# Kernel tuning notes

Measured on AMD Instinct MI355X. Metric: run time of the kernel, lower is better.

## Reference

```python
import jax, jax.numpy as jnp
import numpy as np

DIN = 512      # input feature dim (din)
HEADS = 8
DHEAD = 64
DIM = HEADS * DHEAD  # 512
NTOT = 12288   # total nodes across all graphs
NBATCH = 32    # number of graphs
NMAX = 512     # padded max nodes per graph (<= pf_threshold ~562 -> softmax branch)
EPS = 1e-5


def setup_inputs() -> dict:
    key = jax.random.key(0)
    ks = jax.random.split(key, 7)
    z = jax.random.normal(ks[0], (NTOT, DIN), jnp.float32)
    src = jnp.sort(jax.random.randint(ks[1], (NTOT,), 0, NBATCH)).astype(jnp.int32)
    w_scale = 1.0 / np.sqrt(DIN)
    Wq = jax.random.normal(ks[2], (DIN, DIM), jnp.float32) * w_scale
    Wk = jax.random.normal(ks[3], (DIN, DIM), jnp.float32) * w_scale
    Wv = jax.random.normal(ks[4], (DIN, DIM), jnp.float32) * w_scale
    Wo = jax.random.normal(ks[5], (DIM, DIM), jnp.float32) * w_scale
    bo = jnp.zeros((DIM,), jnp.float32)
    ln_gamma = jnp.ones((DIN,), jnp.float32)
    ln_beta = jnp.zeros((DIN,), jnp.float32)
    return {"z": z, "src": src, "ln_gamma": ln_gamma, "ln_beta": ln_beta,
            "Wq": Wq, "Wk": Wk, "Wv": Wv, "Wo": Wo, "bo": bo,
            "n_max": NMAX, "n_batch": NBATCH}


def reference(z, src, ln_gamma, ln_beta, Wq, Wk, Wv, Wo, bo, n_max, n_batch):
    # --- LayerNorm(din) ---
    mu = jnp.mean(z, axis=-1, keepdims=True)
    var = jnp.mean(jnp.square(z - mu), axis=-1, keepdims=True)
    zn = (z - mu) * jax.lax.rsqrt(var + EPS) * ln_gamma + ln_beta

    # --- to_dense_batch(zn, src): src is sorted graph-id per node ---
    ntot = z.shape[0]
    counts = jnp.bincount(src, length=n_batch)                    # [B]
    starts = jnp.concatenate([jnp.zeros((1,), counts.dtype), jnp.cumsum(counts)[:-1]])
    pos = jnp.arange(ntot) - starts[src]                          # position within graph
    x = jnp.zeros((n_batch, n_max, DIN), zn.dtype).at[src, pos].set(zn)   # [B,N,din]
    mask = jnp.zeros((n_batch, n_max), bool).at[src, pos].set(True)       # [B,N]

    # --- q/k/v projections, split heads: b n (h d) -> b h n d ---
    def heads(t):
        return t.reshape(n_batch, n_max, HEADS, DHEAD).transpose(0, 2, 1, 3)
    q = heads(x @ Wq)
    k = heads(x @ Wk)
    v = heads(x @ Wv)

    # --- manual masked softmax attention (N <= pf_threshold branch) ---
    s = jnp.einsum('bhmd,bhnd->bhmn', q, k)
    s = jnp.where(mask[:, None, None, :], s, -jnp.inf)
    a = jax.nn.softmax(s * (DHEAD ** -0.5), axis=-1)
    o = jnp.einsum('bhmn,bhnd->bhmd', a, v)

    # --- merge heads, gather valid rows (out[mask]), output projection ---
    o = o.transpose(0, 2, 1, 3).reshape(n_batch, n_max, DIM)
    h = o[src, pos] @ Wo + bo                                     # [Ntot, DIM]
    return h
```

## Files before the change

### kernel.cpp

```cpp
#include <hip/hip_runtime.h>
#include <hip/hip_bf16.h>
#include <math.h>

#define DIN 512
#define DIM 512
#define NHEADS 8
#define DHEAD 64
#define NB 32
#define NPAD 512
#define NPTOT (NB * NPAD)

typedef __attribute__((ext_vector_type(8))) short bf16x8;
typedef __attribute__((ext_vector_type(8))) unsigned short u16x8;
typedef __attribute__((ext_vector_type(4))) float f32x4;

typedef __attribute__((address_space(3))) unsigned int lds_u32;
typedef __attribute__((address_space(1))) const unsigned int g_u32;

__device__ __forceinline__ void gll16(const unsigned short* g, unsigned short* l) {
  __builtin_amdgcn_global_load_lds((g_u32*)g, (lds_u32*)l, 16, 0, 0);
}

__device__ inline unsigned short f2bf(float x) {
  unsigned int u = __float_as_uint(x);
  unsigned int r = (u + 0x7FFFu + ((u >> 16) & 1u)) >> 16;
  return (unsigned short)r;
}

__global__ __launch_bounds__(256) void prep_kernel(const float* __restrict__ z,
                                                   const float* __restrict__ gamma,
                                                   const float* __restrict__ beta,
                                                   const int* __restrict__ src,
                                                   const float* __restrict__ Wq,
                                                   const float* __restrict__ Wk,
                                                   const float* __restrict__ Wv,
                                                   const float* __restrict__ Wo,
                                                   unsigned short* __restrict__ zn,
                                                   int* __restrict__ starts,
                                                   int* __restrict__ dstrow,
                                                   unsigned short* __restrict__ WtQKV,
                                                   unsigned short* __restrict__ WtO,
                                                   int ntot) {
  __shared__ float tile[32][33];
  int b = blockIdx.x;
  int nln = ntot >> 2;
  int nmap = (ntot + 255) >> 8;
  if (b < nln) {
    int wave = b * 4 + (threadIdx.x >> 6);
    int lane = threadIdx.x & 63;
    const float* row = z + (size_t)wave * DIN;
    float4 a = ((const float4*)row)[lane];
    float4 bb = ((const float4*)row)[64 + lane];
    float s  = a.x + a.y + a.z + a.w + bb.x + bb.y + bb.z + bb.w;
    float sq = a.x*a.x + a.y*a.y + a.z*a.z + a.w*a.w
             + bb.x*bb.x + bb.y*bb.y + bb.z*bb.z + bb.w*bb.w;
#pragma unroll
    for (int off = 32; off; off >>= 1) {
      s  += __shfl_xor(s, off);
      sq += __shfl_xor(sq, off);
    }
    float mu  = s * (1.0f / DIN);
    float var = sq * (1.0f / DIN) - mu * mu;
    float r   = rsqrtf(var + 1e-5f);
    float4 g0 = ((const float4*)gamma)[lane];
    float4 g1 = ((const float4*)gamma)[64 + lane];
    float4 b0 = ((const float4*)beta)[lane];
    float4 b1 = ((const float4*)beta)[64 + lane];
    ushort4 o0, o1;
    o0.x = f2bf((a.x - mu) * r * g0.x + b0.x);
    o0.y = f2bf((a.y - mu) * r * g0.y + b0.y);
    o0.z = f2bf((a.z - mu) * r * g0.z + b0.z);
    o0.w = f2bf((a.w - mu) * r * g0.w + b0.w);
    o1.x = f2bf((bb.x - mu) * r * g1.x + b1.x);
    o1.y = f2bf((bb.y - mu) * r * g1.y + b1.y);
    o1.z = f2bf((bb.z - mu) * r * g1.z + b1.z);
    o1.w = f2bf((bb.w - mu) * r * g1.w + b1.w);
    ((ushort4*)(zn + (size_t)wave * DIN))[lane] = o0;
    ((ushort4*)(zn + (size_t)wave * DIN))[64 + lane] = o1;
  } else if (b < nln + nmap) {
    int bid = b - nln;
    if (bid == 0 && threadIdx.x <= NB) {
      int gg = threadIdx.x;
      int lo = 0, hi = ntot;
      while (lo < hi) { int mid = (lo + hi) >> 1; if (src[mid] < gg) lo = mid + 1; else hi = mid; }
      starts[gg] = lo;
    }
    int i = bid * 256 + threadIdx.x;
    if (i < ntot) {
      int gg = src[i];
      int lo = 0, hi = ntot;
      while (lo < hi) { int mid = (lo + hi) >> 1; if (src[mid] < gg) lo = mid + 1; else hi = mid; }
      dstrow[i] = gg * NPAD + (i - lo);
    }
  } else {
    int idx = b - nln - nmap;
    int zz = idx >> 8;
    int rem = idx & 255;
    const float* W; unsigned short* Wt;
    if (zz == 0)      { W = Wq; Wt = WtQKV; }
    else if (zz == 1) { W = Wk; Wt = WtQKV + (size_t)512 * DIN; }
    else if (zz == 2) { W = Wv; Wt = WtQKV + (size_t)1024 * DIN; }
    else              { W = Wo; Wt = WtO; }
    int k0 = (rem & 15) * 32;
    int n0 = (rem >> 4) * 32;
    int tx = threadIdx.x & 31;
    int ty = threadIdx.x >> 5;
#pragma unroll
    for (int i = 0; i < 4; i++)
      tile[ty + i * 8][tx] = W[(size_t)(k0 + ty + i * 8) * DIM + n0 + tx];
    __syncthreads();
#pragma unroll
    for (int i = 0; i < 4; i++)
      Wt[(size_t)(n0 + ty + i * 8) * DIN + k0 + tx] = f2bf(tile[tx][ty + i * 8]);
  }
}

template <int NCOLS, bool BIAS, bool OUT_F32, bool REMAP>
__global__ __launch_bounds__(256) void gemm_staged(const unsigned short* __restrict__ A,
                                                   const unsigned short* __restrict__ Bt,
                                                   const float* __restrict__ bias,
                                                   const int* __restrict__ remap,
                                                   unsigned short* __restrict__ Cbf,
                                                   float* __restrict__ Cf) {
  __shared__ unsigned short smem[16384];
  int tid = threadIdx.x, lane = tid & 63, wv = tid >> 6;
  int col = lane & 15, quad = lane >> 4;
  int m0 = blockIdx.x * 128, n0 = blockIdx.y * 128;
  int msub = (wv & 1) * 64, nsub = (wv >> 1) * 64;

  int srow = lane >> 2;
  int cswz = (((lane & 3) ^ ((lane >> 3) & 3))) * 8;

  f32x4 acc[4][4];
#pragma unroll
  for (int i = 0; i < 4; i++)
#pragma unroll
    for (int j = 0; j < 4; j++) acc[i][j] = (f32x4){0.f, 0.f, 0.f, 0.f};

  auto stage = [&](int ks, int nb) {
    const unsigned short* Ab = A  + (size_t)m0 * DIN + ks * 32;
    const unsigned short* Bb = Bt + (size_t)n0 * DIN + ks * 32;
#pragma unroll
    for (int i = 0; i < 2; i++) {
      int t = wv * 2 + i;
      gll16(Ab + (size_t)(t * 16 + srow) * DIN + cswz, smem + nb * 4096 + t * 512);
      gll16(Bb + (size_t)(t * 16 + srow) * DIN + cswz, smem + 8192 + nb * 4096 + t * 512);
    }
  };

  stage(0, 0);
#pragma unroll 2
  for (int ks = 0; ks < 16; ks++) {
    int cur = ks & 1;
    __syncthreads();
    if (ks + 1 < 16) stage(ks + 1, 1 - cur);
    bf16x8 af[4], bfr[4];
#pragma unroll
    for (int mt = 0; mt < 4; mt++) {
      int row = msub + mt * 16 + col;
      af[mt] = *(const bf16x8*)&smem[cur * 4096 + row * 32 + ((quad ^ ((row >> 1) & 3)) * 8)];
    }
#pragma unroll
    for (int nt = 0; nt < 4; nt++) {
      int row = nsub + nt * 16 + col;
      bfr[nt] = *(const bf16x8*)&smem[8192 + cur * 4096 + row * 32 + ((quad ^ ((row >> 1) & 3)) * 8)];
    }
#pragma unroll
    for (int mt = 0; mt < 4; mt++)
#pragma unroll
      for (int nt = 0; nt < 4; nt++)
        acc[mt][nt] = __builtin_amdgcn_mfma_f32_16x16x32_bf16(af[mt], bfr[nt], acc[mt][nt], 0, 0, 0);
  }

  if (!OUT_F32) {
    __syncthreads();
#pragma unroll
    for (int mt = 0; mt < 4; mt++)
#pragma unroll
      for (int r = 0; r < 4; r++) {
        int row = msub + mt * 16 + quad * 4 + r;
#pragma unroll
        for (int nt = 0; nt < 4; nt++) {
          int c = nsub + nt * 16 + col;
          float v = acc[mt][nt][r] + (BIAS ? bias[n0 + c] : 0.f);
          smem[row * 128 + (((c >> 3) ^ (quad << 1)) * 8) + (c & 7)] = f2bf(v);
        }
      }
    __syncthreads();
#pragma unroll
    for (int pass = 0; pass < 8; pass++) {
      int row = pass * 16 + (tid >> 4);
      int sw  = ((row >> 2) & 3) << 1;
      int ch  = tid & 15;
      u16x8 vv = *(const u16x8*)&smem[row * 128 + ((ch ^ sw) * 8)];
      int drow = REMAP ? remap[m0 + row] : (m0 + row);
      *(u16x8*)(Cbf + (size_t)drow * NCOLS + n0 + ch * 8) = vv;
    }
  } else {
    float* smemf = (float*)smem;
    float bv[4];
#pragma unroll
    for (int nt = 0; nt < 4; nt++) bv[nt] = BIAS ? bias[n0 + nsub + nt * 16 + col] : 0.f;
#pragma unroll
    for (int hh = 0; hh < 2; hh++) {
      __syncthreads();
      if ((wv & 1) == hh) {
#pragma unroll
        for (int mt = 0; mt < 4; mt++)
#pragma unroll
          for (int r = 0; r < 4; r++) {
            int row64 = mt * 16 + quad * 4 + r;
#pragma unroll
            for (int nt = 0; nt < 4; nt++) {
              int c = nsub + nt * 16 + col;
              smemf[row64 * 128 + (c ^ (quad * 16))] = acc[mt][nt][r] + bv[nt];
            }
          }
      }
      __syncthreads();
#pragma unroll
      for (int p = 0; p < 2; p++) {
        int row64 = p * 32 + (tid >> 3);
        int sub = tid & 7;
        int sw = ((row64 >> 2) & 3) * 16;
#pragma unroll
        for (int i = 0; i < 4; i++) {
          int c = sub * 4 + i * 32;
          f32x4 v4 = *(const f32x4*)&smemf[row64 * 128 + (c ^ sw)];
          *(f32x4*)&Cf[(size_t)(m0 + hh * 64 + row64) * NCOLS + n0 + c] = v4;
        }
      }
    }
  }
}

__global__ __launch_bounds__(256, 3) void fattn_kernel(const unsigned short* __restrict__ qkvp,
                                                       const int* __restrict__ starts,
                                                       unsigned short* __restrict__ obuf) {
  __shared__ unsigned short Kbuf[2][64 * 64];
  __shared__ unsigned short Vbuf[2][64 * 64];
  __shared__ unsigned short Plds[4][32 * 64];
  int g = blockIdx.x, h = blockIdx.y, qt = blockIdx.z;
  int st = starts[g];
  int n  = starts[g + 1] - st;
  int q0b = qt * 128;
  if (q0b >= n) return;
  int tid = threadIdx.x, lane = tid & 63, wv = tid >> 6;
  int col = lane & 15, quad = lane >> 4;
  int q0 = q0b + wv * 32;
  bool active = q0 < n;
  int ntiles = (n + 63) >> 6;

  bf16x8 qf[2][2];
  if (active) {
#pragma unroll
    for (int a = 0; a < 2; a++) {
      const unsigned short* qp = qkvp + (size_t)(g * NPAD + q0 + a * 16 + col) * 1536 + h * 64 + quad * 8;
      qf[a][0] = *(const bf16x8*)(qp);
      qf[a][1] = *(const bf16x8*)(qp + 32);
    }
  }

  int srow = tid >> 2;
  int sc   = (tid & 3) * 2;
  int kwoff0 = srow * 64 + ((sc ^ (srow & 7)) * 8);
  int kwoff1 = srow * 64 + (((sc + 1) ^ (srow & 7)) * 8);
  int vkp = tid >> 3;
  int vdc = tid & 7;
  int vkc   = vkp >> 2;
  int vkoff = (vkp & 3) * 2;
  u16x8 kreg0, kreg1, vreg0, vreg1;
  auto loadregs = [&](int kt) {
    const unsigned short* kp = qkvp + (size_t)(g * NPAD + kt + srow) * 1536 + 512 + h * 64 + sc * 8;
    kreg0 = *(const u16x8*)(kp);
    kreg1 = *(const u16x8*)(kp + 8);
    const unsigned short* vp = qkvp + (size_t)(g * NPAD + kt + 2 * vkp) * 1536 + 1024 + h * 64 + vdc * 8;
    vreg0 = *(const u16x8*)(vp);
    vreg1 = *(const u16x8*)(vp + 1536);
  };
  auto writelds = [&](int bsel) {
    *(u16x8*)&Kbuf[bsel][kwoff0] = kreg0;
    *(u16x8*)&Kbuf[bsel][kwoff1] = kreg1;
#pragma unroll
    for (int i = 0; i < 8; i++) {
      int d = vdc * 8 + i;
      unsigned int pv = (unsigned int)(unsigned short)vreg0[i]
                      | ((unsigned int)(unsigned short)vreg1[i] << 16);
      *(unsigned int*)&Vbuf[bsel][d * 64 + ((vkc ^ (d & 7) ^ (d >> 3)) * 8) + vkoff] = pv;
    }
  };

  bf16x8 onesv;
#pragma unroll
  for (int i = 0; i < 8; i++) onesv[i] = (short)0x3F80;

  f32x4 oa[2][4];
  f32x4 lacc[2];
#pragma unroll
  for (int a = 0; a < 2; a++) {
    lacc[a] = (f32x4){0.f, 0.f, 0.f, 0.f};
#pragma unroll
    for (int i = 0; i < 4; i++) oa[a][i] = (f32x4){0.f, 0.f, 0.f, 0.f};
  }

  loadregs(0);
  writelds(0);
  __syncthreads();

  for (int t = 0; t < ntiles; t++) {
    int cur = t & 1;
    if (t + 1 < ntiles) loadregs((t + 1) * 64);
    if (active) {
      f32x4 s[2][4];
#pragma unroll
      for (int a = 0; a < 2; a++)
#pragma unroll
        for (int j = 0; j < 4; j++) s[a][j] = (f32x4){0.f, 0.f, 0.f, 0.f};
#pragma unroll
      for (int j = 0; j < 4; j++) {
        int R = j * 16 + col;
        bf16x8 kf0 = *(const bf16x8*)&Kbuf[cur][R * 64 + ((quad ^ (R & 7)) * 8)];
        bf16x8 kf1 = *(const bf16x8*)&Kbuf[cur][R * 64 + (((4 + quad) ^ (R & 7)) * 8)];
        s[0][j] = __builtin_amdgcn_mfma_f32_16x16x32_bf16(qf[0][0], kf0, s[0][j], 0, 0, 0);
        s[0][j] = __builtin_amdgcn_mfma_f32_16x16x32_bf16(qf[0][1], kf1, s[0][j], 0, 0, 0);
        s[1][j] = __builtin_amdgcn_mfma_f32_16x16x32_bf16(qf[1][0], kf0, s[1][j], 0, 0, 0);
        s[1][j] = __builtin_amdgcn_mfma_f32_16x16x32_bf16(qf[1][1], kf1, s[1][j], 0, 0, 0);
      }
      int kt = t * 64;
#pragma unroll
      for (int j = 0; j < 4; j++) {
        bool valid = (kt + j * 16 + col) < n;
#pragma unroll
        for (int a = 0; a < 2; a++)
#pragma unroll
          for (int r = 0; r < 4; r++)
            s[a][j][r] = valid ? __expf(s[a][j][r] * 0.125f) : 0.f;
      }
#pragma unroll
      for (int a = 0; a < 2; a++)
#pragma unroll
        for (int r = 0; r < 4; r++) {
          int R = a * 16 + quad * 4 + r;
#pragma unroll
          for (int j = 0; j < 4; j++) {
            int chunk = j * 2 + (col >> 3);
            Plds[wv][R * 64 + ((chunk ^ (R & 7)) * 8) + (col & 7)] = f2bf(s[a][j][r]);
          }
        }
      __builtin_amdgcn_fence(__ATOMIC_ACQ_REL, "workgroup");
      bf16x8 pf[2][2];
#pragma unroll
      for (int a = 0; a < 2; a++) {
        int R = a * 16 + col;
        pf[a][0] = *(const bf16x8*)&Plds[wv][R * 64 + ((quad ^ (col & 7)) * 8)];
        pf[a][1] = *(const bf16x8*)&Plds[wv][R * 64 + (((4 + quad) ^ (col & 7)) * 8)];
      }
#pragma unroll
      for (int dt = 0; dt < 4; dt++) {
        int R = dt * 16 + col;
        int swz = (R & 7) ^ (R >> 3);
        bf16x8 vf0 = *(const bf16x8*)&Vbuf[cur][R * 64 + ((quad ^ swz) * 8)];
        bf16x8 vf1 = *(const bf16x8*)&Vbuf[cur][R * 64 + (((quad + 4) ^ swz) * 8)];
        oa[0][dt] = __builtin_amdgcn_mfma_f32_16x16x32_bf16(pf[0][0], vf0, oa[0][dt], 0, 0, 0);
        oa[0][dt] = __builtin_amdgcn_mfma_f32_16x16x32_bf16(pf[0][1], vf1, oa[0][dt], 0, 0, 0);
        oa[1][dt] = __builtin_amdgcn_mfma_f32_16x16x32_bf16(pf[1][0], vf0, oa[1][dt], 0, 0, 0);
        oa[1][dt] = __builtin_amdgcn_mfma_f32_16x16x32_bf16(pf[1][1], vf1, oa[1][dt], 0, 0, 0);
      }
      lacc[0] = __builtin_amdgcn_mfma_f32_16x16x32_bf16(pf[0][0], onesv, lacc[0], 0, 0, 0);
      lacc[0] = __builtin_amdgcn_mfma_f32_16x16x32_bf16(pf[0][1], onesv, lacc[0], 0, 0, 0);
      lacc[1] = __builtin_amdgcn_mfma_f32_16x16x32_bf16(pf[1][0], onesv, lacc[1], 0, 0, 0);
      lacc[1] = __builtin_amdgcn_mfma_f32_16x16x32_bf16(pf[1][1], onesv, lacc[1], 0, 0, 0);
    }
    if (t + 1 < ntiles) writelds(1 - cur);
    __syncthreads();
  }

  if (active) {
#pragma unroll
    for (int a = 0; a < 2; a++)
#pragma unroll
      for (int r = 0; r < 4; r++) {
        int q = q0 + a * 16 + quad * 4 + r;
        if (q < n) {
          float inv = 1.0f / lacc[a][r];
          unsigned short* op = obuf + (size_t)(st + q) * DIM + h * 64 + col;
          op[0]  = f2bf(oa[a][0][r] * inv);
          op[16] = f2bf(oa[a][1][r] * inv);
          op[32] = f2bf(oa[a][2][r] * inv);
          op[48] = f2bf(oa[a][3][r] * inv);
        }
      }
  }
}

extern "C" void kernel_launch(void* const* d_in, const int* in_sizes, int n_in,
                              void* d_out, int out_size, void* d_ws, size_t ws_size,
                              hipStream_t stream) {
  const float* z     = (const float*)d_in[0];
  const int*   src   = (const int*)d_in[1];
  const float* gamma = (const float*)d_in[2];
  const float* beta  = (const float*)d_in[3];
  const float* Wq    = (const float*)d_in[4];
  const float* Wk    = (const float*)d_in[5];
  const float* Wv    = (const float*)d_in[6];
  const float* Wo    = (const float*)d_in[7];
  const float* bo    = (const float*)d_in[8];
  int ntot = in_sizes[0] / DIN;
  float* out = (float*)d_out;

  char* ws = (char*)d_ws;
  size_t off = 0;
  unsigned short* zn    = (unsigned short*)(ws + off); off += (size_t)ntot * DIN * 2;
  unsigned short* qkvp  = (unsigned short*)(ws + off); off += (size_t)NPTOT * 1536 * 2;
  unsigned short* obuf  = (unsigned short*)(ws + off); off += (size_t)ntot * DIM * 2;
  unsigned short* WtQKV = (unsigned short*)(ws + off); off += (size_t)1536 * DIN * 2;
  unsigned short* WtO   = (unsigned short*)(ws + off); off += (size_t)DIM * DIN * 2;
  int* starts           = (int*)(ws + off);            off += 64 * 4;
  int* dstrow           = (int*)(ws + off);

  int nln = ntot >> 2;
  int nmap = (ntot + 255) >> 8;
  prep_kernel<<<nln + nmap + 1024, 256, 0, stream>>>(z, gamma, beta, src, Wq, Wk, Wv, Wo,
                                                     zn, starts, dstrow, WtQKV, WtO, ntot);

  gemm_staged<1536, false, false, true>
      <<<dim3(ntot / 128, 12), 256, 0, stream>>>(zn, WtQKV, nullptr, dstrow, qkvp, nullptr);

  fattn_kernel<<<dim3(NB, NHEADS, 4), 256, 0, stream>>>(qkvp, starts, obuf);

  gemm_staged<512, true, true, false>
      <<<dim3(ntot / 128, 4), 256, 0, stream>>>(obuf, WtO, bo, nullptr, nullptr, out);
}
```

Before: 173.0 us.

## Retile QKV GEMM to 128x192 tiles and split out-proj GEMM into 128x64 tiles

The templated GEMM is split into two specialized kernels. The QKV projection now uses 128x192 tiles, giving 768 blocks instead of 1152 and more B reuse per A load, with the epilogue writing bf16 output in three 64-column passes through LDS. The output projection uses narrower 128x64 tiles, doubling its grid to 768 blocks for better CU occupancy, and writes fp32 results straight from registers instead of staging them in LDS. The trade-offs are higher register pressure in the QKV kernel and less coalesced direct stores in the output kernel.

Result: slower. 185.8 us (+7.4%).

```diff
diff --git a/kernel.cpp b/kernel.cpp
--- a/kernel.cpp
+++ b/kernel.cpp
@@ -115,36 +115,37 @@
   }
 }
 
-template <int NCOLS, bool BIAS, bool OUT_F32, bool REMAP>
-__global__ __launch_bounds__(256) void gemm_staged(const unsigned short* __restrict__ A,
+__global__ __launch_bounds__(256, 3) void gemm_qkv(const unsigned short* __restrict__ A,
                                                    const unsigned short* __restrict__ Bt,
-                                                   const float* __restrict__ bias,
                                                    const int* __restrict__ remap,
-                                                   unsigned short* __restrict__ Cbf,
-                                                   float* __restrict__ Cf) {
-  __shared__ unsigned short smem[16384];
+                                                   unsigned short* __restrict__ Cbf) {
+  __shared__ unsigned short smem[20480];
   int tid = threadIdx.x, lane = tid & 63, wv = tid >> 6;
   int col = lane & 15, quad = lane >> 4;
-  int m0 = blockIdx.x * 128, n0 = blockIdx.y * 128;
-  int msub = (wv & 1) * 64, nsub = (wv >> 1) * 64;
+  int m0 = blockIdx.x * 128, n0 = blockIdx.y * 192;
+  int msub = (wv & 1) * 64, nsub = (wv >> 1) * 96;
 
   int srow = lane >> 2;
   int cswz = (((lane & 3) ^ ((lane >> 3) & 3))) * 8;
 
-  f32x4 acc[4][4];
+  f32x4 acc[4][6];
 #pragma unroll
   for (int i = 0; i < 4; i++)
 #pragma unroll
-    for (int j = 0; j < 4; j++) acc[i][j] = (f32x4){0.f, 0.f, 0.f, 0.f};
+    for (int j = 0; j < 6; j++) acc[i][j] = (f32x4){0.f, 0.f, 0.f, 0.f};
 
   auto stage = [&](int ks, int nb) {
     const unsigned short* Ab = A  + (size_t)m0 * DIN + ks * 32;
     const unsigned short* Bb = Bt + (size_t)n0 * DIN + ks * 32;
 #pragma unroll
-    for (int i = 0; i < 2; i++) {
-      int t = wv * 2 + i;
-      gll16(Ab + (size_t)(t * 16 + srow) * DIN + cswz, smem + nb * 4096 + t * 512);
-      gll16(Bb + (size_t)(t * 16 + srow) * DIN + cswz, smem + 8192 + nb * 4096 + t * 512);
+    for (int i = 0; i < 5; i++) {
+      int t = i * 4 + wv;
+      if (t < 8)
+        gll16(Ab + (size_t)(t * 16 + srow) * DIN + cswz, smem + nb * 4096 + t * 512);
+      else {
+        int tb = t - 8;
+        gll16(Bb + (size_t)(tb * 16 + srow) * DIN + cswz, smem + 8192 + nb * 6144 + tb * 512);
+      }
     }
   };
 
@@ -154,84 +155,123 @@
     int cur = ks & 1;
     __syncthreads();
     if (ks + 1 < 16) stage(ks + 1, 1 - cur);
-    bf16x8 af[4], bfr[4];
+    bf16x8 af[4], bfr[6];
 #pragma unroll
     for (int mt = 0; mt < 4; mt++) {
       int row = msub + mt * 16 + col;
       af[mt] = *(const bf16x8*)&smem[cur * 4096 + row * 32 + ((quad ^ ((row >> 1) & 3)) * 8)];
     }
 #pragma unroll
+    for (int nt = 0; nt < 6; nt++) {
+      int row = nsub + nt * 16 + col;
+      bfr[nt] = *(const bf16x8*)&smem[8192 + cur * 6144 + row * 32 + ((quad ^ ((row >> 1) & 3)) * 8)];
+    }
+#pragma unroll
+    for (int mt = 0; mt < 4; mt++)
+#pragma unroll
+      for (int nt = 0; nt < 6; nt++)
+        acc[mt][nt] = __builtin_amdgcn_mfma_f32_16x16x32_bf16(af[mt], bfr[nt], acc[mt][nt], 0, 0, 0);
+  }
+
+#pragma unroll
+  for (int gcol = 0; gcol < 3; gcol++) {
+    __syncthreads();
+#pragma unroll
+    for (int mt = 0; mt < 4; mt++)
+#pragma unroll
+      for (int r = 0; r < 4; r++) {
+        int row = msub + mt * 16 + quad * 4 + r;
+#pragma unroll
+        for (int nt = 0; nt < 6; nt++) {
+          int c = nsub + nt * 16 + col;
+          if ((c >> 6) == gcol) {
+            int cl = c & 63;
+            smem[row * 64 + (((cl >> 3) ^ (row & 7)) * 8) + (cl & 7)] = f2bf(acc[mt][nt][r]);
+          }
+        }
+      }
+    __syncthreads();
+#pragma unroll
+    for (int pass = 0; pass < 4; pass++) {
+      int row = pass * 32 + (tid >> 3);
+      int ch  = tid & 7;
+      u16x8 vv = *(const u16x8*)&smem[row * 64 + ((ch ^ (row & 7)) * 8)];
+      int drow = remap[m0 + row];
+      *(u16x8*)(Cbf + (size_t)drow * 1536 + n0 + gcol * 64 + ch * 8) = vv;
+    }
+  }
+}
+
+__global__ __launch_bounds__(256, 3) void gemm_out(const unsigned short* __restrict__ A,
+                                                   const unsigned short* __restrict__ Bt,
+                                                   const float* __restrict__ bias,
+                                                   float* __restrict__ Cf) {
+  __shared__ unsigned short smem[12288];
+  int tid = threadIdx.x, lane = tid & 63, wv = tid >> 6;
+  int col = lane & 15, quad = lane >> 4;
+  int m0 = blockIdx.x * 128, n0 = blockIdx.y * 64;
+  int msub = wv * 32;
+
+  int srow = lane >> 2;
+  int cswz = (((lane & 3) ^ ((lane >> 3) & 3))) * 8;
+
+  f32x4 acc[2][4];
+#pragma unroll
+  for (int i = 0; i < 2; i++)
+#pragma unroll
+    for (int j = 0; j < 4; j++) acc[i][j] = (f32x4){0.f, 0.f, 0.f, 0.f};
+
+  auto stage = [&](int ks, int nb) {
+    const unsigned short* Ab = A  + (size_t)m0 * DIN + ks * 32;
+    const unsigned short* Bb = Bt + (size_t)n0 * DIN + ks * 32;
+#pragma unroll
+    for (int i = 0; i < 3; i++) {
+      int t = i * 4 + wv;
+      if (t < 8)
+        gll16(Ab + (size_t)(t * 16 + srow) * DIN + cswz, smem + nb * 4096 + t * 512);
+      else {
+        int tb = t - 8;
+        gll16(Bb + (size_t)(tb * 16 + srow) * DIN + cswz, smem + 8192 + nb * 2048 + tb * 512);
+      }
+    }
+  };
+
+  stage(0, 0);
+#pragma unroll 2
+  for (int ks = 0; ks < 16; ks++) {
+    int cur = ks & 1;
+    __syncthreads();
+    if (ks + 1 < 16) stage(ks + 1, 1 - cur);
+    bf16x8 af[2], bfr[4];
+#pragma unroll
+    for (int mt = 0; mt < 2; mt++) {
+      int row = msub + mt * 16 + col;
+      af[mt] = *(const bf16x8*)&smem[cur * 4096 + row * 32 + ((quad ^ ((row >> 1) & 3)) * 8)];
+    }
+#pragma unroll
     for (int nt = 0; nt < 4; nt++) {
-      int row = nsub + nt * 16 + col;
-      bfr[nt] = *(const bf16x8*)&smem[8192 + cur * 4096 + row * 32 + ((quad ^ ((row >> 1) & 3)) * 8)];
-    }
-#pragma unroll
-    for (int mt = 0; mt < 4; mt++)
+      int row = nt * 16 + col;
+      bfr[nt] = *(const bf16x8*)&smem[8192 + cur * 2048 + row * 32 + ((quad ^ ((row >> 1) & 3)) * 8)];
+    }
+#pragma unroll
+    for (int mt = 0; mt < 2; mt++)
 #pragma unroll
       for (int nt = 0; nt < 4; nt++)
         acc[mt][nt] = __builtin_amdgcn_mfma_f32_16x16x32_bf16(af[mt], bfr[nt], acc[mt][nt], 0, 0, 0);
   }
 
-  if (!OUT_F32) {
-    __syncthreads();
-#pragma unroll
-    for (int mt = 0; mt < 4; mt++)
-#pragma unroll
-      for (int r = 0; r < 4; r++) {
-        int row = msub + mt * 16 + quad * 4 + r;
-#pragma unroll
-        for (int nt = 0; nt < 4; nt++) {
-          int c = nsub + nt * 16 + col;
-          float v = acc[mt][nt][r] + (BIAS ? bias[n0 + c] : 0.f);
-          smem[row * 128 + (((c >> 3) ^ (quad << 1)) * 8) + (c & 7)] = f2bf(v);
-        }
-      }
-    __syncthreads();
-#pragma unroll
-    for (int pass = 0; pass < 8; pass++) {
-      int row = pass * 16 + (tid >> 4);
-      int sw  = ((row >> 2) & 3) << 1;
-      int ch  = tid & 15;
-      u16x8 vv = *(const u16x8*)&smem[row * 128 + ((ch ^ sw) * 8)];
-      int drow = REMAP ? remap[m0 + row] : (m0 + row);
-      *(u16x8*)(Cbf + (size_t)drow * NCOLS + n0 + ch * 8) = vv;
-    }
-  } else {
-    float* smemf = (float*)smem;
-    float bv[4];
-#pragma unroll
-    for (int nt = 0; nt < 4; nt++) bv[nt] = BIAS ? bias[n0 + nsub + nt * 16 + col] : 0.f;
-#pragma unroll
-    for (int hh = 0; hh < 2; hh++) {
-      __syncthreads();
-      if ((wv & 1) == hh) {
-#pragma unroll
-        for (int mt = 0; mt < 4; mt++)
-#pragma unroll
-          for (int r = 0; r < 4; r++) {
-            int row64 = mt * 16 + quad * 4 + r;
-#pragma unroll
-            for (int nt = 0; nt < 4; nt++) {
-              int c = nsub + nt * 16 + col;
-              smemf[row64 * 128 + (c ^ (quad * 16))] = acc[mt][nt][r] + bv[nt];
-            }
-          }
-      }
-      __syncthreads();
-#pragma unroll
-      for (int p = 0; p < 2; p++) {
-        int row64 = p * 32 + (tid >> 3);
-        int sub = tid & 7;
-        int sw = ((row64 >> 2) & 3) * 16;
-#pragma unroll
-        for (int i = 0; i < 4; i++) {
-          int c = sub * 4 + i * 32;
-          f32x4 v4 = *(const f32x4*)&smemf[row64 * 128 + (c ^ sw)];
-          *(f32x4*)&Cf[(size_t)(m0 + hh * 64 + row64) * NCOLS + n0 + c] = v4;
-        }
-      }
-    }
-  }
+  float bv[4];
+#pragma unroll
+  for (int nt = 0; nt < 4; nt++) bv[nt] = bias[n0 + nt * 16 + col];
+#pragma unroll
+  for (int mt = 0; mt < 2; mt++)
+#pragma unroll
+    for (int r = 0; r < 4; r++) {
+      int mrow = m0 + msub + mt * 16 + quad * 4 + r;
+#pragma unroll
+      for (int nt = 0; nt < 4; nt++)
+        Cf[(size_t)mrow * DIM + n0 + nt * 16 + col] = acc[mt][nt][r] + bv[nt];
+    }
 }
 
 __global__ __launch_bounds__(256, 3) void fattn_kernel(const unsigned short* __restrict__ qkvp,
@@ -423,11 +463,9 @@
   prep_kernel<<<nln + nmap + 1024, 256, 0, stream>>>(z, gamma, beta, src, Wq, Wk, Wv, Wo,
                                                      zn, starts, dstrow, WtQKV, WtO, ntot);
 
-  gemm_staged<1536, false, false, true>
-      <<<dim3(ntot / 128, 12), 256, 0, stream>>>(zn, WtQKV, nullptr, dstrow, qkvp, nullptr);
+  gemm_qkv<<<dim3(ntot / 128, 8), 256, 0, stream>>>(zn, WtQKV, dstrow, qkvp);
 
   fattn_kernel<<<dim3(NB, NHEADS, 4), 256, 0, stream>>>(qkvp, starts, obuf);
 
-  gemm_staged<512, true, true, false>
-      <<<dim3(ntot / 128, 4), 256, 0, stream>>>(obuf, WtO, bo, nullptr, nullptr, out);
-}
+  gemm_out<<<dim3(ntot / 128, 8), 256, 0, stream>>>(obuf, WtO, bo, out);
+}
```
